# Optimization experiments

Measured on AMD Instinct MI355X. Metric: run time of the kernel, lower is better.

Reference implementation:

```python
import jax, jax.numpy as jnp
import numpy as np

B, P, D, T, O = 32, 2048, 768, 3, 128
H = D // 4  # Head bottleneck dim


def setup_inputs() -> dict:
    key = jax.random.key(0)
    ks = jax.random.split(key, 16)
    s = 0.02  # init_std (trunc_normal approximated by normal*std)
    f32 = jnp.float32
    return {
        "x": jax.random.normal(ks[0], (B, P, D), f32),
        "mask": jax.random.randint(ks[1], (B, P), 0, 2).astype(bool),  # True = masked/invalid
        "task_token": s * jax.random.normal(ks[2], (T, D), f32),
        "Wq": s * jax.random.normal(ks[3], (T, D, D), f32),
        "bq": jnp.zeros((T, D), f32),
        "Wk": s * jax.random.normal(ks[4], (T, D, D), f32),
        "bk": jnp.zeros((T, D), f32),
        "Wv": s * jax.random.normal(ks[5], (T, D, D), f32),
        "bv": jnp.zeros((T, D), f32),
        "Wo": s * jax.random.normal(ks[6], (T, D, D), f32),
        "bo": jnp.zeros((T, D), f32),
        "h1w": s * jax.random.normal(ks[7], (T, D, H), f32),
        "h1b": jnp.zeros((T, H), f32),
        "h2w": s * jax.random.normal(ks[8], (T, H, O), f32),
        "h2b": jnp.zeros((T, O), f32),
    }


def reference(x, mask, task_token, Wq, bq, Wk, bk, Wv, bv, Wo, bo, h1w, h1b, h2w, h2b):
    # Masked cross-attention over valid tokens == gather-valid-then-attend in the torch code.
    scale = 1.0 / jnp.sqrt(jnp.asarray(D, x.dtype))
    q = jnp.einsum('td,tde->te', task_token, Wq) + bq                       # (T,D)
    k = jnp.einsum('bpd,tde->tbpe', x, Wk) + bk[:, None, None, :]           # (T,B,P,D)
    v = jnp.einsum('bpd,tde->tbpe', x, Wv) + bv[:, None, None, :]           # (T,B,P,D)
    scores = jnp.einsum('te,tbpe->tbp', q, k) * scale                       # (T,B,P)
    scores = jnp.where(mask[None, :, :], jnp.asarray(-1e9, scores.dtype), scores)
    attn = jax.nn.softmax(scores, axis=-1)
    y = jnp.einsum('tbp,tbpe->tbe', attn, v)                                # (T,B,D)
    y = jnp.einsum('tbe,tef->tbf', y, Wo) + bo[:, None, :]                  # attn output proj
    y = y + task_token[:, None, :]                                          # residual with task token
    h = jax.nn.gelu(jnp.einsum('tbd,tdh->tbh', y, h1w) + h1b[:, None, :], approximate=False)
    out = jnp.einsum('tbh,tho->tbo', h, h2w) + h2b[:, None, :]              # (T,B,O)
    return out
```

## Files before the change

### kernel.cpp

```cpp
#include <hip/hip_runtime.h>
#include <math.h>

#define BB 32
#define PP 2048
#define DD 768
#define TT 3
#define OO 128
#define HH 192
#define CC 32
#define ROWS (PP / CC)
#define SCALE 0.03608439182435161f

template<int K, int N, int B_, int ECH, int KSP, bool ADD_TT, bool GELU>
__global__ void k_mv(const float* __restrict__ in, const float* __restrict__ W,
                     const float* __restrict__ bias, const float* __restrict__ tt,
                     float* __restrict__ out) {
    __shared__ float red[KSP][ECH];
    constexpr int NCH = N / ECH;
    int blk = blockIdx.x;
    int t = blk / (B_ * NCH);
    int rem = blk % (B_ * NCH);
    int b = rem / NCH;
    int ec = rem % NCH;
    int tid = threadIdx.x;
    int le = tid % ECH;
    int kg = tid / ECH;
    int e = ec * ECH + le;
    const float* inr = in + ((size_t)t * B_ + b) * K;
    const float* wc = W + (size_t)t * K * N + e;
    float acc = 0.f;
    constexpr int KPT = K / KSP;
    int d0 = kg * KPT;
#pragma unroll 8
    for (int d = d0; d < d0 + KPT; ++d)
        acc += inr[d] * wc[(size_t)d * N];
    red[kg][le] = acc;
    __syncthreads();
    if (kg == 0) {
        float s = bias[t * N + e];
        if (ADD_TT) s += tt[t * N + e];
#pragma unroll
        for (int i = 0; i < KSP; ++i) s += red[i][le];
        if (GELU) s = 0.5f * s * (1.0f + erff(s * 0.70710678118654752f));
        out[((size_t)t * B_ + b) * N + e] = s;
    }
}

__global__ void k_kq(const float* __restrict__ Wk, const float* __restrict__ q,
                     float* __restrict__ kq) {
    int t = blockIdx.x / 192;
    int d = (blockIdx.x % 192) * 4 + (threadIdx.x >> 6);
    int L = threadIdx.x & 63;
    const float4* wr = (const float4*)(Wk + (size_t)(t * DD + d) * DD);
    const float4* qr = (const float4*)(q + t * DD);
    float s = 0.f;
#pragma unroll
    for (int g = 0; g < 3; ++g) {
        float4 a = wr[g * 64 + L], b = qr[g * 64 + L];
        s += a.x * b.x + a.y * b.y + a.z * b.z + a.w * b.w;
    }
#pragma unroll
    for (int off = 32; off; off >>= 1) s += __shfl_xor(s, off);
    if (L == 0) kq[t * DD + d] = s * SCALE;
}

__global__ __launch_bounds__(256, 4) void k_main(const float* __restrict__ x,
        const int* __restrict__ mask, const float* __restrict__ kq,
        float* __restrict__ xap, float* __restrict__ lp) {
    __shared__ float red[4][TT * DD];
    __shared__ float redl[4][TT];
    int bid = blockIdx.x;
    int b = bid >> 5, c = bid & 31;
    int tid = threadIdx.x, w = tid >> 6, L = tid & 63;

    float* kqs = &red[0][0];
#pragma unroll
    for (int k2 = 0; k2 < 9; ++k2) kqs[tid + k2 * 256] = kq[tid + k2 * 256];
    __syncthreads();
    const float4* kq4 = (const float4*)kqs;

    float4 acc[TT][3] = {};
    float l[TT] = {0.f, 0.f, 0.f};
    const float* xb = x + (size_t)b * PP * DD;
    const int* mb = mask + b * PP;
    int p0 = c * ROWS + w * (ROWS / 4);

    for (int r = 0; r < ROWS / 4; ++r) {
        int p = p0 + r;
        if (mb[p]) continue;
        const float4* xr = (const float4*)(xb + (size_t)p * DD);
        float4 xv[3];
#pragma unroll
        for (int g = 0; g < 3; ++g) xv[g] = xr[g * 64 + L];
        float s[TT];
#pragma unroll
        for (int t = 0; t < TT; ++t) {
            float a = 0.f;
#pragma unroll
            for (int g = 0; g < 3; ++g) {
                float4 kf = kq4[t * 192 + g * 64 + L];
                a += xv[g].x * kf.x + xv[g].y * kf.y
                   + xv[g].z * kf.z + xv[g].w * kf.w;
            }
            s[t] = a;
        }
#pragma unroll
        for (int off = 32; off; off >>= 1) {
            s[0] += __shfl_xor(s[0], off);
            s[1] += __shfl_xor(s[1], off);
            s[2] += __shfl_xor(s[2], off);
        }
#pragma unroll
        for (int t = 0; t < TT; ++t) {
            float e = expf(s[t]);
            l[t] += e;
#pragma unroll
            for (int g = 0; g < 3; ++g) {
                acc[t][g].x += e * xv[g].x;
                acc[t][g].y += e * xv[g].y;
                acc[t][g].z += e * xv[g].z;
                acc[t][g].w += e * xv[g].w;
            }
        }
    }

    __syncthreads();
#pragma unroll
    for (int t = 0; t < TT; ++t)
#pragma unroll
        for (int g = 0; g < 3; ++g)
            *(float4*)&red[w][t * DD + g * 256 + 4 * L] = acc[t][g];
    if (L == 0) {
#pragma unroll
        for (int t = 0; t < TT; ++t) redl[w][t] = l[t];
    }
    __syncthreads();

    float* outp = xap + (size_t)bid * (TT * DD);
#pragma unroll
    for (int k = 0; k < 9; ++k) {
        int i = tid + k * 256;
        outp[i] = red[0][i] + red[1][i] + red[2][i] + red[3][i];
    }
    if (tid < TT)
        lp[bid * TT + tid] = redl[0][tid] + redl[1][tid] + redl[2][tid] + redl[3][tid];
}

__global__ void k_comb(const float* __restrict__ xap, const float* __restrict__ lp,
                       float* __restrict__ xa) {
    int t = blockIdx.x >> 5, b = blockIdx.x & 31;
    int tid = threadIdx.x;
    float lsum = 0.f;
#pragma unroll
    for (int c = 0; c < CC; ++c) lsum += lp[(b * CC + c) * TT + t];
    float inv = 1.0f / lsum;
#pragma unroll
    for (int k = 0; k < 3; ++k) {
        int d = tid + k * 256;
        float s = 0.f;
#pragma unroll
        for (int c = 0; c < CC; ++c)
            s += xap[(size_t)(b * CC + c) * (TT * DD) + t * DD + d];
        xa[(t * BB + b) * DD + d] = s * inv;
    }
}

extern "C" void kernel_launch(void* const* d_in, const int* in_sizes, int n_in,
                              void* d_out, int out_size, void* d_ws, size_t ws_size,
                              hipStream_t stream) {
    const float* x    = (const float*)d_in[0];
    const int*   mask = (const int*)d_in[1];
    const float* tt   = (const float*)d_in[2];
    const float* Wq   = (const float*)d_in[3];
    const float* bq   = (const float*)d_in[4];
    const float* Wk   = (const float*)d_in[5];
    const float* Wv   = (const float*)d_in[7];
    const float* bv   = (const float*)d_in[8];
    const float* Wo   = (const float*)d_in[9];
    const float* bo   = (const float*)d_in[10];
    const float* h1w  = (const float*)d_in[11];
    const float* h1b  = (const float*)d_in[12];
    const float* h2w  = (const float*)d_in[13];
    const float* h2b  = (const float*)d_in[14];
    float* out = (float*)d_out;

    float* ws  = (float*)d_ws;
    float* q   = ws;
    float* kq  = q + TT * DD;
    float* xap = kq + TT * DD;
    float* lp  = xap + BB * CC * TT * DD;
    float* xa  = lp + BB * CC * TT;
    float* y   = xa + TT * BB * DD;
    float* y2  = y + TT * BB * DD;
    float* h   = y2 + TT * BB * DD;

    hipLaunchKernelGGL((k_mv<DD, DD, 1, 64, 16, false, false>),
                       dim3(TT * 12), dim3(1024), 0, stream, tt, Wq, bq, nullptr, q);
    hipLaunchKernelGGL(k_kq,   dim3(576),  dim3(256), 0, stream, Wk, q, kq);
    hipLaunchKernelGGL(k_main, dim3(BB * CC), dim3(256), 0, stream, x, mask, kq, xap, lp);
    hipLaunchKernelGGL(k_comb, dim3(96),   dim3(256), 0, stream, xap, lp, xa);
    hipLaunchKernelGGL((k_mv<DD, DD, BB, 64, 4, false, false>),
                       dim3(TT * BB * 12), dim3(256), 0, stream, xa, Wv, bv, nullptr, y);
    hipLaunchKernelGGL((k_mv<DD, DD, BB, 64, 4, true, false>),
                       dim3(TT * BB * 12), dim3(256), 0, stream, y, Wo, bo, tt, y2);
    hipLaunchKernelGGL((k_mv<DD, HH, BB, 64, 4, false, true>),
                       dim3(TT * BB * 3), dim3(256), 0, stream, y2, h1w, h1b, nullptr, h);
    hipLaunchKernelGGL((k_mv<HH, OO, BB, 128, 2, false, false>),
                       dim3(TT * BB * 1), dim3(256), 0, stream, h, h2w, h2b, nullptr, out);
}
```

Baseline: 102.3 us.

## Batch weight reuse across B in post-attention GEMVs with split-K partials

```diff
diff --git a/kernel.cpp b/kernel.cpp
--- a/kernel.cpp
+++ b/kernel.cpp
@@ -11,38 +11,26 @@
 #define ROWS (PP / CC)
 #define SCALE 0.03608439182435161f
 
-template<int K, int N, int B_, int ECH, int KSP, bool ADD_TT, bool GELU>
-__global__ void k_mv(const float* __restrict__ in, const float* __restrict__ W,
-                     const float* __restrict__ bias, const float* __restrict__ tt,
-                     float* __restrict__ out) {
-    __shared__ float red[KSP][ECH];
-    constexpr int NCH = N / ECH;
-    int blk = blockIdx.x;
-    int t = blk / (B_ * NCH);
-    int rem = blk % (B_ * NCH);
-    int b = rem / NCH;
-    int ec = rem % NCH;
-    int tid = threadIdx.x;
-    int le = tid % ECH;
-    int kg = tid / ECH;
-    int e = ec * ECH + le;
-    const float* inr = in + ((size_t)t * B_ + b) * K;
-    const float* wc = W + (size_t)t * K * N + e;
-    float acc = 0.f;
-    constexpr int KPT = K / KSP;
-    int d0 = kg * KPT;
-#pragma unroll 8
-    for (int d = d0; d < d0 + KPT; ++d)
-        acc += inr[d] * wc[(size_t)d * N];
-    red[kg][le] = acc;
+__global__ void k_q(const float* __restrict__ tt, const float* __restrict__ Wq,
+                    const float* __restrict__ bq, float* __restrict__ q) {
+    __shared__ float red[16][16];
+    int t = blockIdx.x / 48, ec = blockIdx.x % 48;
+    int tid = threadIdx.x;
+    int le = tid & 15, kg = tid >> 4;
+    int e = ec * 16 + le;
+    const float* w  = Wq + (size_t)t * DD * DD + e;
+    const float* tr = tt + t * DD;
+    float a = 0.f;
+#pragma unroll 4
+    for (int d = kg * 48; d < kg * 48 + 48; ++d)
+        a += tr[d] * w[(size_t)d * DD];
+    red[kg][le] = a;
     __syncthreads();
     if (kg == 0) {
-        float s = bias[t * N + e];
-        if (ADD_TT) s += tt[t * N + e];
-#pragma unroll
-        for (int i = 0; i < KSP; ++i) s += red[i][le];
-        if (GELU) s = 0.5f * s * (1.0f + erff(s * 0.70710678118654752f));
-        out[((size_t)t * B_ + b) * N + e] = s;
+        float s = bq[t * DD + e];
+#pragma unroll
+        for (int i = 0; i < 16; ++i) s += red[i][le];
+        q[t * DD + e] = s;
     }
 }
 
@@ -162,6 +150,81 @@
         for (int c = 0; c < CC; ++c)
             s += xap[(size_t)(b * CC + c) * (TT * DD) + t * DD + d];
         xa[(t * BB + b) * DD + d] = s * inv;
+    }
+}
+
+template<int K, int N, int KC>
+__global__ void k_p1(const float* __restrict__ in, const float* __restrict__ W,
+                     float* __restrict__ part) {
+    constexpr int KCH = K / KC;
+    constexpr int NCH = N / 64;
+    __shared__ float ins[BB][KCH];
+    int blk = blockIdx.x;
+    int t  = blk / (KC * NCH);
+    int r  = blk % (KC * NCH);
+    int kc = r / NCH;
+    int ec = r % NCH;
+    int tid = threadIdx.x;
+
+    constexpr int TOT = BB * KCH;
+    for (int i = tid; i < TOT; i += 256) {
+        int b = i / KCH, kk = i % KCH;
+        ins[b][kk] = in[((size_t)t * BB + b) * K + kc * KCH + kk];
+    }
+    __syncthreads();
+
+    int le = tid & 63, bg = tid >> 6;
+    int e = ec * 64 + le;
+    const float* wp = W + (size_t)t * K * N + (size_t)(kc * KCH) * N + e;
+    float acc[8] = {};
+#pragma unroll 4
+    for (int kk = 0; kk < KCH; ++kk) {
+        float wv = wp[(size_t)kk * N];
+#pragma unroll
+        for (int j = 0; j < 8; ++j)
+            acc[j] += ins[bg * 8 + j][kk] * wv;
+    }
+#pragma unroll
+    for (int j = 0; j < 8; ++j)
+        part[(((size_t)t * KC + kc) * BB + (bg * 8 + j)) * N + e] = acc[j];
+}
+
+template<int N, int KC, bool ADD_TT, bool GELU>
+__global__ void k_p2(const float* __restrict__ part, const float* __restrict__ bias,
+                     const float* __restrict__ tt, float* __restrict__ out) {
+    int t = blockIdx.x / BB, b = blockIdx.x % BB;
+    int tid = threadIdx.x;
+    for (int e = tid; e < N; e += 256) {
+        float s = bias[t * N + e];
+        if (ADD_TT) s += tt[t * N + e];
+#pragma unroll
+        for (int kc = 0; kc < KC; ++kc)
+            s += part[(((size_t)t * KC + kc) * BB + b) * N + e];
+        if (GELU) s = 0.5f * s * (1.0f + erff(s * 0.70710678118654752f));
+        out[((size_t)t * BB + b) * N + e] = s;
+    }
+}
+
+__global__ void k_tail(const float* __restrict__ partH, const float* __restrict__ h1b,
+                       const float* __restrict__ h2w, const float* __restrict__ h2b,
+                       float* __restrict__ out) {
+    __shared__ float hl[HH];
+    int t = blockIdx.x / BB, b = blockIdx.x % BB;
+    int tid = threadIdx.x;
+    if (tid < HH) {
+        float s = h1b[t * HH + tid];
+#pragma unroll
+        for (int kc = 0; kc < 8; ++kc)
+            s += partH[(((size_t)t * 8 + kc) * BB + b) * HH + tid];
+        hl[tid] = 0.5f * s * (1.0f + erff(s * 0.70710678118654752f));
+    }
+    __syncthreads();
+    if (tid < OO) {
+        float s = h2b[t * OO + tid];
+#pragma unroll 8
+        for (int kh = 0; kh < HH; ++kh)
+            s += hl[kh] * h2w[((size_t)t * HH + kh) * OO + tid];
+        out[((size_t)t * BB + b) * OO + tid] = s;
     }
 }
 
@@ -184,27 +247,26 @@
     const float* h2b  = (const float*)d_in[14];
     float* out = (float*)d_out;
 
-    float* ws  = (float*)d_ws;
-    float* q   = ws;
-    float* kq  = q + TT * DD;
-    float* xap = kq + TT * DD;
-    float* lp  = xap + BB * CC * TT * DD;
-    float* xa  = lp + BB * CC * TT;
-    float* y   = xa + TT * BB * DD;
-    float* y2  = y + TT * BB * DD;
-    float* h   = y2 + TT * BB * DD;
-
-    hipLaunchKernelGGL((k_mv<DD, DD, 1, 64, 16, false, false>),
-                       dim3(TT * 12), dim3(1024), 0, stream, tt, Wq, bq, nullptr, q);
-    hipLaunchKernelGGL(k_kq,   dim3(576),  dim3(256), 0, stream, Wk, q, kq);
+    float* ws    = (float*)d_ws;
+    float* q     = ws;
+    float* kq    = q + TT * DD;
+    float* xap   = kq + TT * DD;
+    float* lp    = xap + BB * CC * TT * DD;
+    float* xa    = lp + BB * CC * TT;
+    float* partV = xa + TT * BB * DD;
+    float* y     = partV + TT * 8 * BB * DD;
+    float* partO = y + TT * BB * DD;
+    float* y2    = partO + TT * 8 * BB * DD;
+    float* partH = y2 + TT * BB * DD;
+
+    hipLaunchKernelGGL(k_q,    dim3(TT * 48), dim3(256), 0, stream, tt, Wq, bq, q);
+    hipLaunchKernelGGL(k_kq,   dim3(576),     dim3(256), 0, stream, Wk, q, kq);
     hipLaunchKernelGGL(k_main, dim3(BB * CC), dim3(256), 0, stream, x, mask, kq, xap, lp);
-    hipLaunchKernelGGL(k_comb, dim3(96),   dim3(256), 0, stream, xap, lp, xa);
-    hipLaunchKernelGGL((k_mv<DD, DD, BB, 64, 4, false, false>),
-                       dim3(TT * BB * 12), dim3(256), 0, stream, xa, Wv, bv, nullptr, y);
-    hipLaunchKernelGGL((k_mv<DD, DD, BB, 64, 4, true, false>),
-                       dim3(TT * BB * 12), dim3(256), 0, stream, y, Wo, bo, tt, y2);
-    hipLaunchKernelGGL((k_mv<DD, HH, BB, 64, 4, false, true>),
-                       dim3(TT * BB * 3), dim3(256), 0, stream, y2, h1w, h1b, nullptr, h);
-    hipLaunchKernelGGL((k_mv<HH, OO, BB, 128, 2, false, false>),
-                       dim3(TT * BB * 1), dim3(256), 0, stream, h, h2w, h2b, nullptr, out);
-}
+    hipLaunchKernelGGL(k_comb, dim3(96),      dim3(256), 0, stream, xap, lp, xa);
+    hipLaunchKernelGGL((k_p1<DD, DD, 8>), dim3(TT * 8 * 12), dim3(256), 0, stream, xa, Wv, partV);
+    hipLaunchKernelGGL((k_p2<DD, 8, false, false>), dim3(TT * BB), dim3(256), 0, stream, partV, bv, nullptr, y);
+    hipLaunchKernelGGL((k_p1<DD, DD, 8>), dim3(TT * 8 * 12), dim3(256), 0, stream, y, Wo, partO);
+    hipLaunchKernelGGL((k_p2<DD, 8, true, false>), dim3(TT * BB), dim3(256), 0, stream, partO, bo, tt, y2);
+    hipLaunchKernelGGL((k_p1<DD, HH, 8>), dim3(TT * 8 * 3), dim3(256), 0, stream, y2, h1w, partH);
+    hipLaunchKernelGGL(k_tail, dim3(TT * BB), dim3(192), 0, stream, partH, h1b, h2w, h2b, out);
+}
```

Measured after the change: 110.9 us. +8.4%, slower.
